# Performance work log

Measured on AMD Instinct MI355X. Metric: run time of the kernel, lower is better.

## Reference

```python
import jax, jax.numpy as jnp
import numpy as np

B, P, S, D, H, DFF, F, FIN = 16, 25, 1024, 128, 8, 512, 1, 4
SIGMA, OMEGA = 0.1, 0.5
DH = D // H


def setup_inputs() -> dict:
    key = jax.random.key(0)
    ks = jax.random.split(key, 16)
    s = lambda i, sh, sc=1.0: jax.random.normal(ks[i], sh, dtype=jnp.float32) * sc
    return dict(
        x=s(0, (B, P, D)),
        y=s(1, (B, FIN, 1)),
        K=s(2, (B, P, S, D), 0.02),
        V=s(3, (B, P, S, D), 0.02),
        w=jnp.ones((B, P, 1), jnp.float32) / P,
        I=jax.random.randint(ks[4], (B, P, S), 0, P, dtype=jnp.int32),
        Wq=s(5, (D, D), 0.05), Wk=s(6, (D, D), 0.05),
        Wv=s(7, (D, D), 0.05), Wo=s(8, (D, D), 0.05),
        W1=s(9, (D, DFF), 0.05), b1=jnp.zeros((DFF,), jnp.float32),
        W2=s(10, (DFF, D), 0.05), b2=jnp.zeros((D,), jnp.float32),
        Wout=s(11, (D, F), 0.05), bout=jnp.zeros((F,), jnp.float32),
        eps_k=s(12, (B, P, 1, D)), eps_v=s(13, (B, P, 1, D)), eps_z=s(14, (B, P, 1, D)),
        t=512,
    )


def reference(x, y, K, V, w, I, Wq, Wk, Wv, Wo, W1, b1, W2, b2, Wout, bout,
              eps_k, eps_v, eps_z, t):
    # ---- MultiHeadAttention_SMC: per-particle self-attention with reparam noise ----
    xq = x[:, :, None, :]                                   # (B,P,1,D)
    q = xq @ Wq                                             # (B,P,1,D)
    k = xq @ Wk + SIGMA * eps_k                             # noisy key particle
    v = xq @ Wv + SIGMA * eps_v                             # noisy value particle
    K = K.at[:, :, t, :].set(k[:, :, 0, :])                 # write current step into state
    V = V.at[:, :, t, :].set(v[:, :, 0, :])
    q_h = q.reshape(B, P, 1, H, DH)
    K_h = K.reshape(B, P, S, H, DH)
    V_h = V.reshape(B, P, S, H, DH)
    scores = jnp.einsum('bpqhd,bpshd->bphqs', q_h, K_h) / jnp.sqrt(jnp.float32(DH))
    valid = (jnp.arange(S) <= t)[None, None, None, None, :]  # attend to steps <= t
    scores = jnp.where(valid, scores, jnp.float32(-1e9))
    attn = jax.nn.softmax(scores, axis=-1)                  # (B,P,H,1,S)
    ctx = jnp.einsum('bphqs,bpshd->bpqhd', attn, V_h).reshape(B, P, 1, D)
    z = ctx @ Wo + SIGMA * eps_z                            # reparametrized attention output

    # ---- FFN + output layer (dropout is identity at inference) ----
    r_ = jax.nn.relu(z @ W1 + b1) @ W2 + b2                 # (B,P,1,D)
    pred = r_ @ Wout + bout                                 # (B,P,1,F)

    p_t = pred[:, :, 0, :]                                  # (B,P,F)
    y_sq = y[..., 0]                                        # (B,FIN)
    y_t = jnp.broadcast_to(y_sq[:, None, 0:1], (B, P, F))   # target_feature = 0
    mu = y_t - p_t                                          # (B,P,F)
    log_w_full = jnp.einsum('bpf,bqf->bpq', mu, mu) * (-0.5 * OMEGA)
    log_w = jnp.diagonal(log_w_full, axis1=1, axis2=2)      # (B,P)
    log_w = log_w - jnp.min(log_w, axis=-1, keepdims=True)
    w_new = jnp.exp(log_w)
    w_new = w_new / jnp.sum(w_new, axis=1, keepdims=True)
    w_new = jax.lax.stop_gradient(w_new)

    # ---- particle resampling: categorical sample + gather on particle axis ----
    idx = jax.random.categorical(jax.random.key(42),
                                 jnp.log(w_new + 1e-10)[:, None, :],
                                 axis=-1, shape=(B, P))     # (B,P) ancestor indices
    K_res = jnp.take_along_axis(K, idx[:, :, None, None], axis=1)
    V_res = jnp.take_along_axis(V, idx[:, :, None, None], axis=1)
    I_res = jnp.take_along_axis(I, idx[:, :, None], axis=1)
    I_new = I_res.at[:, :, t].set(idx.astype(I.dtype))
    return (r_, z, pred, w_new[..., None], K_res, V_res, I_new)
```

## Files before the change

kernel.cpp:

```cpp
#include <hip/hip_runtime.h>
#include <math.h>

#define B_ 16
#define P_ 25
#define S_ 1024
#define D_ 128
#define H_ 8
#define DH_ 16
#define DFF_ 512
#define SIGMA_ 0.1f

typedef float f4 __attribute__((ext_vector_type(4)));


__global__ __launch_bounds__(128) void qkv_kernel(
    const float* __restrict__ x, const float* __restrict__ Wq,
    const float* __restrict__ Wk, const float* __restrict__ Wv,
    const float* __restrict__ eps_k, const float* __restrict__ eps_v,
    float* __restrict__ q, float* __restrict__ k, float* __restrict__ v) {
  int bp = blockIdx.x;
  int d = threadIdx.x;
  __shared__ float xs[D_];
  xs[d] = x[bp * D_ + d];
  __syncthreads();
  float accq = 0.f, acck = 0.f, accv = 0.f;
  for (int i = 0; i < D_; ++i) {
    float xv = xs[i];
    accq += xv * Wq[i * D_ + d];
    acck += xv * Wk[i * D_ + d];
    accv += xv * Wv[i * D_ + d];
  }
  q[bp * D_ + d] = accq;
  k[bp * D_ + d] = acck + SIGMA_ * eps_k[bp * D_ + d];
  v[bp * D_ + d] = accv + SIGMA_ * eps_v[bp * D_ + d];
}

__global__ __launch_bounds__(512) void attn_kernel(
    const float* __restrict__ q, const float* __restrict__ kn,
    const float* __restrict__ vn, const float* __restrict__ K,
    const float* __restrict__ V, const int* __restrict__ tptr,
    float* __restrict__ ctx) {
  int bp = blockIdx.x;
  int t = tptr[0];
  int tid = threadIdx.x;
  int wave = tid >> 6;
  int lane = tid & 63;
  int row = lane >> 5;
  int lr = lane & 31;
  int w16 = wave * 2 + row;
  __shared__ __align__(16) float qs[D_];
  __shared__ __align__(16) float accs[16][D_];
  __shared__ float ms[16][H_];
  __shared__ float ls[16][H_];
  if (tid < D_) qs[tid] = q[bp * D_ + tid] * 0.25f;
  __syncthreads();
  const f4* Kb = (const f4*)(K + (size_t)bp * S_ * D_);
  const f4* Vb = (const f4*)(V + (size_t)bp * S_ * D_);
  const f4* kn4 = (const f4*)(kn + bp * D_);
  const f4* vn4 = (const f4*)(vn + bp * D_);
  f4 qv = *(const f4*)(qs + 4 * lr);
  float m = -1e30f, l = 0.f;
  f4 acc = {0.f, 0.f, 0.f, 0.f};
  const int RD4 = D_ / 4;
  for (int s = w16; s <= t; s += 16) {
    const f4 *Kr, *Vr;
    if (s == t) { Kr = kn4; Vr = vn4; }
    else        { Kr = Kb + (size_t)s * RD4; Vr = Vb + (size_t)s * RD4; }
    f4 kk = Kr[lr];
    f4 vv = Vr[lr];
    float p = qv.x * kk.x + qv.y * kk.y + qv.z * kk.z + qv.w * kk.w;
    p += __shfl_xor(p, 1);
    p += __shfl_xor(p, 2);
    float mnew = fmaxf(m, p);
    float scale = expf(m - mnew);
    float e = expf(p - mnew);
    l = l * scale + e;
    acc.x = acc.x * scale + e * vv.x;
    acc.y = acc.y * scale + e * vv.y;
    acc.z = acc.z * scale + e * vv.z;
    acc.w = acc.w * scale + e * vv.w;
    m = mnew;
  }
  *(f4*)(&accs[w16][4 * lr]) = acc;
  if ((lr & 3) == 0) { ms[w16][lr >> 2] = m; ls[w16][lr >> 2] = l; }
  __syncthreads();
  if (tid < D_) {
    int h = tid >> 4;
    float mg = -1e30f;
    for (int w2 = 0; w2 < 16; ++w2) mg = fmaxf(mg, ms[w2][h]);
    float L = 0.f, C = 0.f;
    for (int w2 = 0; w2 < 16; ++w2) {
      float sc = expf(ms[w2][h] - mg);
      L += ls[w2][h] * sc;
      C += accs[w2][tid] * sc;
    }
    ctx[bp * D_ + tid] = C / L;
  }
}

__global__ __launch_bounds__(512) void head_kernel(
    const float* __restrict__ ctx, const float* __restrict__ Wo,
    const float* __restrict__ eps_z, const float* __restrict__ W1,
    const float* __restrict__ b1, const float* __restrict__ W2,
    const float* __restrict__ b2, const float* __restrict__ Wout,
    const float* __restrict__ bout, float* __restrict__ out_r,
    float* __restrict__ out_z, float* __restrict__ out_pred) {
  int bp = blockIdx.x;
  int tid = threadIdx.x;
  int d = tid & 127;
  int qq = tid >> 7;
  __shared__ float cs[D_];
  __shared__ float zs[D_];
  __shared__ float as_[DFF_];
  __shared__ float rs[D_];
  __shared__ float part[4][D_];
  if (tid < D_) cs[tid] = ctx[bp * D_ + tid];
  __syncthreads();
  {
    float acc = 0.f;
    int i0 = qq * 32;
    for (int i = i0; i < i0 + 32; ++i) acc += cs[i] * Wo[i * D_ + d];
    part[qq][d] = acc;
  }
  __syncthreads();
  if (tid < D_) {
    float z = part[0][tid] + part[1][tid] + part[2][tid] + part[3][tid] +
              SIGMA_ * eps_z[bp * D_ + tid];
    zs[tid] = z;
    out_z[bp * D_ + tid] = z;
  }
  __syncthreads();
  {
    float acc = b1[tid];
    for (int i = 0; i < D_; ++i) acc += zs[i] * W1[i * DFF_ + tid];
    as_[tid] = fmaxf(acc, 0.f);
  }
  __syncthreads();
  {
    float acc = 0.f;
    int j0 = qq * 128;
    for (int j = j0; j < j0 + 128; ++j) acc += as_[j] * W2[j * D_ + d];
    part[qq][d] = acc;
  }
  __syncthreads();
  if (tid < D_) {
    float r = part[0][tid] + part[1][tid] + part[2][tid] + part[3][tid] + b2[tid];
    rs[tid] = r;
    out_r[bp * D_ + tid] = r;
  }
  __syncthreads();
  if (tid < 64) {
    float acc = rs[tid] * Wout[tid] + rs[tid + 64] * Wout[tid + 64];
    acc += __shfl_xor(acc, 1);
    acc += __shfl_xor(acc, 2);
    acc += __shfl_xor(acc, 4);
    acc += __shfl_xor(acc, 8);
    acc += __shfl_xor(acc, 16);
    acc += __shfl_xor(acc, 32);
    if (tid == 0) out_pred[bp] = acc + bout[0];
  }
}

__device__ inline unsigned rotl_(unsigned x, int r) {
  return (x << r) | (x >> (32 - r));
}

__device__ inline void threefry2x32_(unsigned x0, unsigned x1, unsigned& o0,
                                     unsigned& o1) {
  const unsigned k0 = 0u, k1 = 42u;
  const unsigned k2 = k0 ^ k1 ^ 0x1BD11BDAu;
  x0 += k0; x1 += k1;
#define RND_(r) { x0 += x1; x1 = rotl_(x1, r); x1 ^= x0; }
  RND_(13) RND_(15) RND_(26) RND_(6)   x0 += k1; x1 += k2 + 1u;
  RND_(17) RND_(29) RND_(16) RND_(24)  x0 += k2; x1 += k0 + 2u;
  RND_(13) RND_(15) RND_(26) RND_(6)   x0 += k0; x1 += k1 + 3u;
  RND_(17) RND_(29) RND_(16) RND_(24)  x0 += k1; x1 += k2 + 4u;
  RND_(13) RND_(15) RND_(26) RND_(6)   x0 += k2; x1 += k0 + 5u;
#undef RND_
  o0 = x0; o1 = x1;
}

__device__ inline float gumbel_at_(int n) {
  unsigned o0, o1;
  threefry2x32_(0u, (unsigned)n, o0, o1);
  unsigned bits = o0 ^ o1;
  unsigned fb = (bits >> 9) | 0x3f800000u;
  float f = __uint_as_float(fb) - 1.0f;
  const float tiny = 1.1754944e-38f;
  float u = fmaxf(tiny, f * (1.0f - tiny) + tiny);
  return -logf(-logf(u));
}

__global__ __launch_bounds__(64) void sample_kernel(
    const float* __restrict__ pred, const float* __restrict__ y,
    float* __restrict__ out_w, int* __restrict__ idx) {
  int b = blockIdx.x;
  int tid = threadIdx.x;
  __shared__ float lw[P_];
  __shared__ float logits[P_];
  __shared__ float red[2];
  if (tid < P_) {
    float mu = y[b * 4] - pred[b * P_ + tid];
    lw[tid] = -0.25f * (mu * mu);
  }
  __syncthreads();
  if (tid == 0) {
    float mn = lw[0];
    for (int p = 1; p < P_; ++p) mn = fminf(mn, lw[p]);
    red[0] = mn;
  }
  __syncthreads();
  if (tid < P_) lw[tid] = expf(lw[tid] - red[0]);
  __syncthreads();
  if (tid == 0) {
    float s = 0.f;
    for (int p = 0; p < P_; ++p) s += lw[p];
    red[1] = s;
  }
  __syncthreads();
  if (tid < P_) {
    float wn = lw[tid] / red[1];
    out_w[b * P_ + tid] = wn;
    logits[tid] = logf(wn + 1e-10f);
  }
  __syncthreads();
  if (tid < P_) {
    float best = -1e30f;
    int bestj = 0;
    for (int j = 0; j < P_; ++j) {
      int n = (b * P_ + tid) * P_ + j;
      float val = gumbel_at_(n) + logits[j];
      if (val > best) { best = val; bestj = j; }
    }
    idx[b * P_ + tid] = bestj;
  }
}

__global__ __launch_bounds__(256) void gather_kernel(
    const float* __restrict__ K, const float* __restrict__ V,
    const float* __restrict__ kn, const float* __restrict__ vn,
    const int* __restrict__ idx, const int* __restrict__ tptr,
    float* __restrict__ outK, float* __restrict__ outV) {
  const int CH = 4;
  const int F4 = (S_ * D_ / 4) / CH;
  int bid = blockIdx.x;
  int tv = bid / (B_ * P_ * CH);
  int rem = bid - tv * (B_ * P_ * CH);
  int bp = rem / CH;
  int chunk = rem - bp * CH;
  int b = bp / P_;
  int j = idx[bp];
  int t = tptr[0];
  const float* src = (tv == 0 ? K : V) + (size_t)(b * P_ + j) * (S_ * D_);
  const f4* sub = (const f4*)((tv == 0 ? kn : vn) + (b * P_ + j) * D_);
  float* dst = (tv == 0 ? outK : outV) + (size_t)bp * (S_ * D_);
  const f4* src4 = (const f4*)src;
  f4* dst4 = (f4*)dst;
  int base = chunk * F4;
  int tlo = t * (D_ / 4);
  for (int i = base + threadIdx.x; i < base + F4; i += 256) {
    f4 val;
    if (i >= tlo && i < tlo + D_ / 4) val = sub[i - tlo];
    else                              val = src4[i];
    __builtin_nontemporal_store(val, dst4 + i);
  }
}

__global__ __launch_bounds__(256) void inew_kernel(
    const int* __restrict__ I, const int* __restrict__ idx,
    const int* __restrict__ tptr, float* __restrict__ outI) {
  int bp = blockIdx.x;
  int b = bp / P_;
  int j = idx[bp];
  int t = tptr[0];
  const int* src = I + (b * P_ + j) * S_;
  float* dst = outI + bp * S_;
  for (int s = threadIdx.x; s < S_; s += 256) {
    int val = (s == t) ? j : src[s];
    __builtin_nontemporal_store((float)val, dst + s);
  }
}

extern "C" void kernel_launch(void* const* d_in, const int* in_sizes, int n_in,
                              void* d_out, int out_size, void* d_ws,
                              size_t ws_size, hipStream_t stream) {
  const float* x     = (const float*)d_in[0];
  const float* y     = (const float*)d_in[1];
  const float* K     = (const float*)d_in[2];
  const float* V     = (const float*)d_in[3];
  const int*   I     = (const int*)d_in[5];
  const float* Wq    = (const float*)d_in[6];
  const float* Wk    = (const float*)d_in[7];
  const float* Wv    = (const float*)d_in[8];
  const float* Wo    = (const float*)d_in[9];
  const float* W1    = (const float*)d_in[10];
  const float* b1    = (const float*)d_in[11];
  const float* W2    = (const float*)d_in[12];
  const float* b2    = (const float*)d_in[13];
  const float* Wout  = (const float*)d_in[14];
  const float* bout  = (const float*)d_in[15];
  const float* eps_k = (const float*)d_in[16];
  const float* eps_v = (const float*)d_in[17];
  const float* eps_z = (const float*)d_in[18];
  const int*   tptr  = (const int*)d_in[19];

  float* out      = (float*)d_out;
  float* out_r    = out;
  float* out_z    = out + 51200;
  float* out_pred = out + 102400;
  float* out_w    = out + 102800;
  float* outK     = out + 103200;
  float* outV     = outK + (size_t)52428800;
  float* outI     = outV + (size_t)52428800;

  float* ws  = (float*)d_ws;
  float* q   = ws;
  float* k   = ws + 51200;
  float* v   = ws + 102400;
  float* ctx = ws + 153600;
  int*   idx = (int*)(ws + 204800);

  qkv_kernel<<<B_ * P_, 128, 0, stream>>>(x, Wq, Wk, Wv, eps_k, eps_v, q, k, v);
  attn_kernel<<<B_ * P_, 512, 0, stream>>>(q, k, v, K, V, tptr, ctx);
  head_kernel<<<B_ * P_, 512, 0, stream>>>(ctx, Wo, eps_z, W1, b1, W2, b2, Wout,
                                           bout, out_r, out_z, out_pred);
  sample_kernel<<<B_, 64, 0, stream>>>(out_pred, y, out_w, idx);
  gather_kernel<<<B_ * P_ * 4 * 2, 256, 0, stream>>>(K, V, k, v, idx, tptr,
                                                     outK, outV);
  inew_kernel<<<B_ * P_, 256, 0, stream>>>(I, idx, tptr, outI);
}
```

Before: 814.5 us.

## Fuse qkv, attention and head kernels; merge gather with index update

Merges the QKV projection, attention and FFN/output head into one per-particle kernel, so q and ctx stay in shared memory and no longer round-trip through global memory. The gather and I-update kernels become one launch. The goal is fewer launches and less intermediate traffic. The gather also switches from nontemporal stores to normal stores for the large K/V copy, which can change cache behaviour on the dominant memory-bound copy.

Result: faster. 779.3 us (-4.3%).

```diff
diff --git a/kernel.cpp b/kernel.cpp
--- a/kernel.cpp
+++ b/kernel.cpp
@@ -13,77 +13,99 @@
 typedef float f4 __attribute__((ext_vector_type(4)));
 
 
-__global__ __launch_bounds__(128) void qkv_kernel(
+__global__ __launch_bounds__(512) void fused_kernel(
     const float* __restrict__ x, const float* __restrict__ Wq,
     const float* __restrict__ Wk, const float* __restrict__ Wv,
     const float* __restrict__ eps_k, const float* __restrict__ eps_v,
-    float* __restrict__ q, float* __restrict__ k, float* __restrict__ v) {
+    const float* __restrict__ K, const float* __restrict__ V,
+    const int* __restrict__ tptr, const float* __restrict__ Wo,
+    const float* __restrict__ eps_z, const float* __restrict__ W1,
+    const float* __restrict__ b1, const float* __restrict__ W2,
+    const float* __restrict__ b2, const float* __restrict__ Wout,
+    const float* __restrict__ bout, float* __restrict__ kw,
+    float* __restrict__ vw, float* __restrict__ out_r,
+    float* __restrict__ out_z, float* __restrict__ out_pred) {
   int bp = blockIdx.x;
-  int d = threadIdx.x;
-  __shared__ float xs[D_];
-  xs[d] = x[bp * D_ + d];
-  __syncthreads();
-  float accq = 0.f, acck = 0.f, accv = 0.f;
-  for (int i = 0; i < D_; ++i) {
-    float xv = xs[i];
-    accq += xv * Wq[i * D_ + d];
-    acck += xv * Wk[i * D_ + d];
-    accv += xv * Wv[i * D_ + d];
-  }
-  q[bp * D_ + d] = accq;
-  k[bp * D_ + d] = acck + SIGMA_ * eps_k[bp * D_ + d];
-  v[bp * D_ + d] = accv + SIGMA_ * eps_v[bp * D_ + d];
-}
-
-__global__ __launch_bounds__(512) void attn_kernel(
-    const float* __restrict__ q, const float* __restrict__ kn,
-    const float* __restrict__ vn, const float* __restrict__ K,
-    const float* __restrict__ V, const int* __restrict__ tptr,
-    float* __restrict__ ctx) {
-  int bp = blockIdx.x;
+  int tid = threadIdx.x;
   int t = tptr[0];
-  int tid = threadIdx.x;
-  int wave = tid >> 6;
-  int lane = tid & 63;
-  int row = lane >> 5;
-  int lr = lane & 31;
-  int w16 = wave * 2 + row;
+
+  __shared__ __align__(16) float xs[D_];
   __shared__ __align__(16) float qs[D_];
+  __shared__ __align__(16) float ks[D_];
+  __shared__ __align__(16) float vs[D_];
   __shared__ __align__(16) float accs[16][D_];
   __shared__ float ms[16][H_];
   __shared__ float ls[16][H_];
-  if (tid < D_) qs[tid] = q[bp * D_ + tid] * 0.25f;
-  __syncthreads();
-  const f4* Kb = (const f4*)(K + (size_t)bp * S_ * D_);
-  const f4* Vb = (const f4*)(V + (size_t)bp * S_ * D_);
-  const f4* kn4 = (const f4*)(kn + bp * D_);
-  const f4* vn4 = (const f4*)(vn + bp * D_);
-  f4 qv = *(const f4*)(qs + 4 * lr);
-  float m = -1e30f, l = 0.f;
-  f4 acc = {0.f, 0.f, 0.f, 0.f};
-  const int RD4 = D_ / 4;
-  for (int s = w16; s <= t; s += 16) {
-    const f4 *Kr, *Vr;
-    if (s == t) { Kr = kn4; Vr = vn4; }
-    else        { Kr = Kb + (size_t)s * RD4; Vr = Vb + (size_t)s * RD4; }
-    f4 kk = Kr[lr];
-    f4 vv = Vr[lr];
-    float p = qv.x * kk.x + qv.y * kk.y + qv.z * kk.z + qv.w * kk.w;
-    p += __shfl_xor(p, 1);
-    p += __shfl_xor(p, 2);
-    float mnew = fmaxf(m, p);
-    float scale = expf(m - mnew);
-    float e = expf(p - mnew);
-    l = l * scale + e;
-    acc.x = acc.x * scale + e * vv.x;
-    acc.y = acc.y * scale + e * vv.y;
-    acc.z = acc.z * scale + e * vv.z;
-    acc.w = acc.w * scale + e * vv.w;
-    m = mnew;
-  }
-  *(f4*)(&accs[w16][4 * lr]) = acc;
-  if ((lr & 3) == 0) { ms[w16][lr >> 2] = m; ls[w16][lr >> 2] = l; }
-  __syncthreads();
+  __shared__ float cs[D_];
+  __shared__ float zs[D_];
+  __shared__ float as_[DFF_];
+  __shared__ float rs[D_];
+  __shared__ float part[4][D_];
+
+  if (tid < D_) xs[tid] = x[bp * D_ + tid];
+  __syncthreads();
+
+  {
+    int mat = tid >> 7;
+    int d = tid & 127;
+    if (mat < 3) {
+      const float* W = (mat == 0) ? Wq : (mat == 1) ? Wk : Wv;
+      float acc = 0.f;
+      for (int i = 0; i < D_; ++i) acc += xs[i] * W[i * D_ + d];
+      if (mat == 0) {
+        qs[d] = acc * 0.25f;
+      } else if (mat == 1) {
+        float kk = acc + SIGMA_ * eps_k[bp * D_ + d];
+        ks[d] = kk;
+        kw[bp * D_ + d] = kk;
+      } else {
+        float vv = acc + SIGMA_ * eps_v[bp * D_ + d];
+        vs[d] = vv;
+        vw[bp * D_ + d] = vv;
+      }
+    }
+  }
+  __syncthreads();
+
+  {
+    int wave = tid >> 6;
+    int lane = tid & 63;
+    int row = lane >> 5;
+    int lr = lane & 31;
+    int w16 = wave * 2 + row;
+    const f4* Kb = (const f4*)(K + (size_t)bp * S_ * D_);
+    const f4* Vb = (const f4*)(V + (size_t)bp * S_ * D_);
+    f4 qv = *(const f4*)(qs + 4 * lr);
+    float m = -1e30f, l = 0.f;
+    f4 acc = {0.f, 0.f, 0.f, 0.f};
+    const int RD4 = D_ / 4;
+    for (int s = w16; s <= t; s += 16) {
+      f4 kk, vv;
+      if (s == t) {
+        kk = *(const f4*)(ks + 4 * lr);
+        vv = *(const f4*)(vs + 4 * lr);
+      } else {
+        kk = Kb[(size_t)s * RD4 + lr];
+        vv = Vb[(size_t)s * RD4 + lr];
+      }
+      float p = qv.x * kk.x + qv.y * kk.y + qv.z * kk.z + qv.w * kk.w;
+      p += __shfl_xor(p, 1);
+      p += __shfl_xor(p, 2);
+      float mnew = fmaxf(m, p);
+      float scale = expf(m - mnew);
+      float e = expf(p - mnew);
+      l = l * scale + e;
+      acc.x = acc.x * scale + e * vv.x;
+      acc.y = acc.y * scale + e * vv.y;
+      acc.z = acc.z * scale + e * vv.z;
+      acc.w = acc.w * scale + e * vv.w;
+      m = mnew;
+    }
+    *(f4*)(&accs[w16][4 * lr]) = acc;
+    if ((lr & 3) == 0) { ms[w16][lr >> 2] = m; ls[w16][lr >> 2] = l; }
+  }
+  __syncthreads();
+
   if (tid < D_) {
     int h = tid >> 4;
     float mg = -1e30f;
@@ -94,28 +116,12 @@
       L += ls[w2][h] * sc;
       C += accs[w2][tid] * sc;
     }
-    ctx[bp * D_ + tid] = C / L;
-  }
-}
-
-__global__ __launch_bounds__(512) void head_kernel(
-    const float* __restrict__ ctx, const float* __restrict__ Wo,
-    const float* __restrict__ eps_z, const float* __restrict__ W1,
-    const float* __restrict__ b1, const float* __restrict__ W2,
-    const float* __restrict__ b2, const float* __restrict__ Wout,
-    const float* __restrict__ bout, float* __restrict__ out_r,
-    float* __restrict__ out_z, float* __restrict__ out_pred) {
-  int bp = blockIdx.x;
-  int tid = threadIdx.x;
+    cs[tid] = C / L;
+  }
+  __syncthreads();
+
   int d = tid & 127;
   int qq = tid >> 7;
-  __shared__ float cs[D_];
-  __shared__ float zs[D_];
-  __shared__ float as_[DFF_];
-  __shared__ float rs[D_];
-  __shared__ float part[4][D_];
-  if (tid < D_) cs[tid] = ctx[bp * D_ + tid];
-  __syncthreads();
   {
     float acc = 0.f;
     int i0 = qq * 32;
@@ -239,45 +245,44 @@
 __global__ __launch_bounds__(256) void gather_kernel(
     const float* __restrict__ K, const float* __restrict__ V,
     const float* __restrict__ kn, const float* __restrict__ vn,
-    const int* __restrict__ idx, const int* __restrict__ tptr,
-    float* __restrict__ outK, float* __restrict__ outV) {
+    const int* __restrict__ I, const int* __restrict__ idx,
+    const int* __restrict__ tptr, float* __restrict__ outK,
+    float* __restrict__ outV, float* __restrict__ outI) {
   const int CH = 4;
   const int F4 = (S_ * D_ / 4) / CH;
+  const int NG = B_ * P_ * CH * 2;
   int bid = blockIdx.x;
-  int tv = bid / (B_ * P_ * CH);
-  int rem = bid - tv * (B_ * P_ * CH);
-  int bp = rem / CH;
-  int chunk = rem - bp * CH;
-  int b = bp / P_;
-  int j = idx[bp];
   int t = tptr[0];
-  const float* src = (tv == 0 ? K : V) + (size_t)(b * P_ + j) * (S_ * D_);
-  const f4* sub = (const f4*)((tv == 0 ? kn : vn) + (b * P_ + j) * D_);
-  float* dst = (tv == 0 ? outK : outV) + (size_t)bp * (S_ * D_);
-  const f4* src4 = (const f4*)src;
-  f4* dst4 = (f4*)dst;
-  int base = chunk * F4;
-  int tlo = t * (D_ / 4);
-  for (int i = base + threadIdx.x; i < base + F4; i += 256) {
-    f4 val;
-    if (i >= tlo && i < tlo + D_ / 4) val = sub[i - tlo];
-    else                              val = src4[i];
-    __builtin_nontemporal_store(val, dst4 + i);
-  }
-}
-
-__global__ __launch_bounds__(256) void inew_kernel(
-    const int* __restrict__ I, const int* __restrict__ idx,
-    const int* __restrict__ tptr, float* __restrict__ outI) {
-  int bp = blockIdx.x;
-  int b = bp / P_;
-  int j = idx[bp];
-  int t = tptr[0];
-  const int* src = I + (b * P_ + j) * S_;
-  float* dst = outI + bp * S_;
-  for (int s = threadIdx.x; s < S_; s += 256) {
-    int val = (s == t) ? j : src[s];
-    __builtin_nontemporal_store((float)val, dst + s);
+  if (bid < NG) {
+    int tv = bid / (B_ * P_ * CH);
+    int rem = bid - tv * (B_ * P_ * CH);
+    int bp = rem / CH;
+    int chunk = rem - bp * CH;
+    int b = bp / P_;
+    int j = idx[bp];
+    const float* src = (tv == 0 ? K : V) + (size_t)(b * P_ + j) * (S_ * D_);
+    const f4* sub = (const f4*)((tv == 0 ? kn : vn) + (b * P_ + j) * D_);
+    float* dst = (tv == 0 ? outK : outV) + (size_t)bp * (S_ * D_);
+    const f4* src4 = (const f4*)src;
+    f4* dst4 = (f4*)dst;
+    int base = chunk * F4;
+    int tlo = t * (D_ / 4);
+    for (int i = base + threadIdx.x; i < base + F4; i += 256) {
+      f4 val;
+      if (i >= tlo && i < tlo + D_ / 4) val = sub[i - tlo];
+      else                              val = src4[i];
+      dst4[i] = val;
+    }
+  } else {
+    int bp = bid - NG;
+    int b = bp / P_;
+    int j = idx[bp];
+    const int* src = I + (b * P_ + j) * S_;
+    float* dst = outI + bp * S_;
+    for (int s = threadIdx.x; s < S_; s += 256) {
+      int val = (s == t) ? j : src[s];
+      dst[s] = (float)val;
+    }
   }
 }
 
@@ -314,18 +319,14 @@
   float* outI     = outV + (size_t)52428800;
 
   float* ws  = (float*)d_ws;
-  float* q   = ws;
-  float* k   = ws + 51200;
-  float* v   = ws + 102400;
-  float* ctx = ws + 153600;
-  int*   idx = (int*)(ws + 204800);
-
-  qkv_kernel<<<B_ * P_, 128, 0, stream>>>(x, Wq, Wk, Wv, eps_k, eps_v, q, k, v);
-  attn_kernel<<<B_ * P_, 512, 0, stream>>>(q, k, v, K, V, tptr, ctx);
-  head_kernel<<<B_ * P_, 512, 0, stream>>>(ctx, Wo, eps_z, W1, b1, W2, b2, Wout,
-                                           bout, out_r, out_z, out_pred);
+  float* k   = ws;
+  float* v   = ws + 51200;
+  int*   idx = (int*)(ws + 102400);
+
+  fused_kernel<<<B_ * P_, 512, 0, stream>>>(
+      x, Wq, Wk, Wv, eps_k, eps_v, K, V, tptr, Wo, eps_z, W1, b1, W2, b2,
+      Wout, bout, k, v, out_r, out_z, out_pred);
   sample_kernel<<<B_, 64, 0, stream>>>(out_pred, y, out_w, idx);
-  gather_kernel<<<B_ * P_ * 4 * 2, 256, 0, stream>>>(K, V, k, v, idx, tptr,
-                                                     outK, outV);
-  inew_kernel<<<B_ * P_, 256, 0, stream>>>(I, idx, tptr, outI);
-}
+  gather_kernel<<<B_ * P_ * 4 * 2 + B_ * P_, 256, 0, stream>>>(
+      K, V, k, v, I, idx, tptr, outK, outV, outI);
+}
```
